# Kernel tuning notes

Measured on AMD Instinct MI355X. Metric: run time of the kernel, lower is better.

Reference implementation:

```python
import jax, jax.numpy as jnp
import numpy as np

B, S, D_MODEL = 1, 1024, 1024
D_CKV, D_CQ = 256, 512
N_HEAD, D_HEAD, D_ROPE = 8, 64, 32


def setup_inputs() -> dict:
    key = jax.random.key(0)
    ks = jax.random.split(key, 12)
    def w(k, shape):
        return jax.random.normal(k, shape, dtype=jnp.float32) * 0.02
    return {
        "x": jax.random.normal(ks[0], (B, S, D_MODEL), dtype=jnp.float32),
        "w_q_idx": w(ks[1], (D_MODEL, N_HEAD * D_HEAD)),
        "w_k_idx": w(ks[2], (D_MODEL, D_HEAD)),
        "w_idx": jnp.ones((N_HEAD,), dtype=jnp.float32),
        "raw_delta": jnp.zeros((D_ROPE // 2,), dtype=jnp.float32),
        "w_dkv": w(ks[3], (D_MODEL, D_CKV)),
        "w_uk": w(ks[4], (D_CKV, N_HEAD * D_HEAD)),
        "w_uv": w(ks[5], (D_CKV, N_HEAD * D_HEAD)),
        "w_dq": w(ks[6], (D_MODEL, D_CQ)),
        "w_uq": w(ks[7], (D_CQ, N_HEAD * D_HEAD)),
        "w_qr": w(ks[8], (D_CQ, N_HEAD * D_ROPE)),
        "w_kr": w(ks[9], (D_MODEL, D_ROPE)),
        "w_out": w(ks[10], (N_HEAD * D_HEAD, D_MODEL)),
        "k_ts": 128,
        "local_window": 64,
    }


def _pope(x, raw_delta, theta):
    # x: (b, L, H, d_rope); positions run along axis 1 (matches torch PoPE)
    delta = -2.0 * jnp.pi * jax.nn.sigmoid(raw_delta)            # (d2,)
    pos = jnp.arange(x.shape[1], dtype=x.dtype)
    ang = pos[None, :, None, None] * theta + delta               # (1, L, 1, d2)
    c, s = jnp.cos(ang), jnp.sin(ang)
    mu1, mu2 = jnp.split(jax.nn.softplus(x), 2, axis=-1)
    return jnp.concatenate((mu1 * c - mu2 * s, mu1 * s + mu2 * c), axis=-1)


def reference(x, w_q_idx, w_k_idx, w_idx, raw_delta, w_dkv, w_uk, w_uv,
              w_dq, w_uq, w_qr, w_kr, w_out, k_ts, local_window):
    b, s, _ = x.shape
    h, dh, dr = N_HEAD, D_HEAD, D_ROPE
    theta = 1.0 / (10000.0 ** (2.0 * jnp.arange(dr // 2, dtype=jnp.float32) / dr))

    # ---- LightningIndexer: per-head relu'd relevance, combined with learned head weights
    qI = (x @ w_q_idx).reshape(b, s, h, dh)
    kI = x @ w_k_idx                                             # (b, s, dh)
    sc = jax.nn.relu(jnp.einsum('bthd,bsd->bths', qI, kI))
    I = jnp.einsum('bths,h->bts', sc, w_idx)

    # ---- TokenSelector: force local window in, mask future out, top-k indices
    qp = jnp.arange(s)[:, None]
    kp = jnp.arange(s)[None, :]
    local = (kp >= qp - local_window + 1) & (kp <= qp)
    causal = kp > qp
    I = jnp.where(local, jnp.inf, I)
    I = jnp.where(causal, -jnp.inf, I)
    k = min(k_ts, s)
    _, idx = jax.lax.top_k(I, k)                                 # (b, s, k) int32

    gather = jax.vmap(lambda t, i: t[i])                         # (s,d),(l,k)->(l,k,d)

    # ---- MLA latent KV, gathered per query
    c_kv = x @ w_dkv                                             # (b, s, d_ckv)
    ckv_sel = gather(c_kv, idx)                                  # (b, s, k, d_ckv)
    key_c = (ckv_sel @ w_uk).reshape(b, s, k, h, dh).transpose(0, 3, 1, 2, 4)
    value = (ckv_sel @ w_uv).reshape(b, s, k, h, dh).transpose(0, 3, 1, 2, 4)

    c_q = x @ w_dq
    query_c = (c_q @ w_uq).reshape(b, s, h, dh).transpose(0, 2, 1, 3)
    query_r = _pope((c_q @ w_qr).reshape(b, s, h, dr), raw_delta, theta).transpose(0, 2, 1, 3)

    # key rope: PoPE applied with positions along the k (selected-token) axis,
    # exactly as the torch code's permute(0,2,1,3) does
    x_sel = gather(x, idx)                                       # (b, s, k, d_model)
    kr = _pope((x_sel @ w_kr).transpose(0, 2, 1, 3), raw_delta, theta).transpose(0, 2, 1, 3)
    key_r = jnp.broadcast_to(kr[:, None], (b, h, s, k, dr))

    query = jnp.concatenate((query_c, query_r), axis=-1)         # (b, h, s, dh+dr)
    keyt = jnp.concatenate((key_c, key_r), axis=-1)              # (b, h, s, k, dh+dr)
    scale = (dh + dr) ** -0.5
    scores = jnp.einsum('bhld,bhlkd->bhlk', query, keyt) * scale
    attn = jax.nn.softmax(scores, axis=-1)
    out = jnp.einsum('bhlk,bhlkd->bhld', attn, value)
    out = out.transpose(0, 2, 1, 3).reshape(b, s, h * dh)
    return out @ w_out
```

## Files before the change

kernel.cpp:

```cpp
#include <hip/hip_runtime.h>
#include <math.h>

#define S_LEN 1024
#define NH 8

typedef __attribute__((ext_vector_type(8))) short bf16x8;
typedef __attribute__((ext_vector_type(4))) float f32x4;

__device__ __forceinline__ float sp_softplus(float x) {
    return fmaxf(x, 0.f) + log1pf(expf(-fabsf(x)));
}

__device__ __forceinline__ unsigned short bfu(float f) {
    unsigned u = __float_as_uint(f);
    unsigned r = (u + 0x7FFFu + ((u >> 16) & 1u)) >> 16;
    return (unsigned short)r;
}

struct FRONT {
    const float *x, *wqidx, *wkidx, *raw_delta, *wuk;
    const float *wdkv, *wdq, *wkr, *wuq, *wqr, *wuv, *wout;
    float *qIP, *kIP, *csc, *css;
    unsigned short *wdkvT, *wdqT, *wkrT, *wuqT, *wqrT, *wuvT, *woutT, *wukb;
};

__global__ __launch_bounds__(256) void front_kernel(FRONT f)
{
    __shared__ float As[2][16][18];
    __shared__ float Bs[2][16][68];
    __shared__ unsigned short tile[64][65];
    int bx = blockIdx.x;
    if (bx < 1152) {
        int gx = bx % 18, gy = bx / 18;
        int half = threadIdx.x >> 7;
        int t = threadIdx.x & 127;
        int u = gx * 2 + half;
        const float* B; float* C;
        int ldb, N, n0, kb;
        if (u < 32) {
            B = f.wqidx; ldb = 512; N = 512;
            C = f.qIP + (long)(u >> 3) * 524288;
            n0 = (u & 7) * 64;
            kb = (u >> 3) * 256;
        } else {
            B = f.wkidx; ldb = 64; N = 64;
            C = f.kIP + (long)(u - 32) * 65536;
            n0 = 0;
            kb = (u - 32) * 256;
        }
        int ke = kb + 256;
        int m0 = gy * 16;
        int ar = t >> 2, ak = t & 3;
        int bk = t >> 3, bn = t & 7;
        int ty = t >> 4, tx = t & 15;

        float4 aN = make_float4(0.f, 0.f, 0.f, 0.f);
        if (t < 64) aN = *(const float4*)(f.x + (long)(m0 + ar) * 1024 + kb + ak * 4);
        float4 b0 = *(const float4*)(B + (long)(kb + bk) * ldb + n0 + bn * 4);
        float4 b1 = *(const float4*)(B + (long)(kb + bk) * ldb + n0 + (bn + 8) * 4);
        float acc[2][4] = {};
        for (int k0 = kb; k0 < ke; k0 += 16) {
            if (t < 64) {
                As[half][ak * 4 + 0][ar] = aN.x;
                As[half][ak * 4 + 1][ar] = aN.y;
                As[half][ak * 4 + 2][ar] = aN.z;
                As[half][ak * 4 + 3][ar] = aN.w;
            }
            *(float4*)&Bs[half][bk][bn * 4] = b0;
            *(float4*)&Bs[half][bk][(bn + 8) * 4] = b1;
            __syncthreads();
            if (k0 + 16 < ke) {
                if (t < 64) aN = *(const float4*)(f.x + (long)(m0 + ar) * 1024 + (k0 + 16) + ak * 4);
                b0 = *(const float4*)(B + (long)(k0 + 16 + bk) * ldb + n0 + bn * 4);
                b1 = *(const float4*)(B + (long)(k0 + 16 + bk) * ldb + n0 + (bn + 8) * 4);
            }
            #pragma unroll
            for (int kk = 0; kk < 16; ++kk) {
                float2 a = *(float2*)&As[half][kk][ty * 2];
                float4 b = *(float4*)&Bs[half][kk][tx * 4];
                acc[0][0] += a.x * b.x; acc[0][1] += a.x * b.y;
                acc[0][2] += a.x * b.z; acc[0][3] += a.x * b.w;
                acc[1][0] += a.y * b.x; acc[1][1] += a.y * b.y;
                acc[1][2] += a.y * b.z; acc[1][3] += a.y * b.w;
            }
            __syncthreads();
        }
        #pragma unroll
        for (int i = 0; i < 2; ++i) {
            float4 v = make_float4(acc[i][0], acc[i][1], acc[i][2], acc[i][3]);
            *(float4*)(C + (long)(m0 + ty * 2 + i) * N + n0 + tx * 4) = v;
        }
    } else if (bx < 1616) {
        int b = bx - 1152;
        const float* srcs[7] = {f.wdkv, f.wdq, f.wkr, f.wuq, f.wqr, f.wuv, f.wout};
        unsigned short* dsts[7] = {f.wdkvT, f.wdqT, f.wkrT, f.wuqT, f.wqrT, f.wuvT, f.woutT};
        const int Ns[7]   = {256, 512, 32, 512, 256, 512, 1024};
        const int Klds[7] = {1024, 1024, 1024, 512, 512, 256, 512};
        const int Ntl[7]  = {4, 8, 1, 8, 4, 8, 16};
        const int bst[8]  = {0, 64, 192, 208, 272, 304, 336, 464};
        int e = 0;
        #pragma unroll
        for (int i = 1; i < 7; ++i) if (b >= bst[i]) e = i;
        int lb = b - bst[e];
        int nt = lb % Ntl[e], kt = lb / Ntl[e];
        const float* src = srcs[e];
        unsigned short* dst = dsts[e];
        int N = Ns[e], Kld = Klds[e];
        int k0 = kt * 64, n0 = nt * 64;
        int t = threadIdx.x;
        int c = t & 63, r4 = t >> 6;
        #pragma unroll
        for (int it = 0; it < 16; ++it) {
            int r = it * 4 + r4;
            float v = (n0 + c < N) ? src[(long)(k0 + r) * N + n0 + c] : 0.f;
            tile[r][c] = bfu(v);
        }
        __syncthreads();
        int wq = t & 7;
        #pragma unroll
        for (int itw = 0; itw < 2; ++itw) {
            int wr = itw * 32 + (t >> 3);
            if (n0 + wr < N) {
                unsigned short v[8];
                #pragma unroll
                for (int j = 0; j < 8; ++j) v[j] = tile[wq * 8 + j][wr];
                *(uint4*)(dst + (long)(n0 + wr) * Kld + k0 + wq * 8) = *(uint4*)v;
            }
        }
    } else if (bx < 1624) {
        int idx = (bx - 1616) * 256 + threadIdx.x;
        int j = idx >> 4, i = idx & 15;
        float rd = f.raw_delta[i];
        float delta = -6.283185307179586f * (1.f / (1.f + expf(-rd)));
        float th = exp2f(-(float)i * 0.83048202372184f);
        float ang = (float)j * th + delta;
        float sv, cv;
        sincosf(ang, &sv, &cv);
        f.csc[idx] = cv;
        f.css[idx] = sv;
    } else {
        int idx = (bx - 1624) * 256 + threadIdx.x;
        f.wukb[idx] = bfu(f.wuk[idx]);
    }
}

struct MFG {
    const float* A[10]; const unsigned short* B[10]; float* C[10];
    int lda[10], ldb[10], ldc[10], K[10], N[10], obf[10];
    int tstart[11]; int ne;
};

__global__ __launch_bounds__(256) void mgemm(MFG mg)
{
    int bx = blockIdx.x, e = 0;
    #pragma unroll
    for (int i = 1; i < 10; ++i) if (i < mg.ne && bx >= mg.tstart[i]) e = i;
    const float* A = mg.A[e];
    const unsigned short* B = mg.B[e];
    float* C = mg.C[e];
    int lda = mg.lda[e], ldb = mg.ldb[e], ldc = mg.ldc[e];
    int K = mg.K[e], N = mg.N[e];
    int m0 = blockIdx.y * 64, n0 = (bx - mg.tstart[e]) * 64;

    __shared__ unsigned short As[64][40];
    __shared__ unsigned short Bs[64][40];
    int t = threadIdx.x;
    int srow = t >> 2, skq = t & 3;
    int wid = t >> 6, l = t & 63;
    int wm = (wid >> 1) * 32, wn = (wid & 1) * 32;
    int fr = l & 15, fk = (l >> 4) * 8;
    bool bok = (n0 + srow) < N;

    f32x4 acc00 = {0.f, 0.f, 0.f, 0.f};
    f32x4 acc01 = {0.f, 0.f, 0.f, 0.f};
    f32x4 acc10 = {0.f, 0.f, 0.f, 0.f};
    f32x4 acc11 = {0.f, 0.f, 0.f, 0.f};

    for (int k0 = 0; k0 < K; k0 += 32) {
        {
            const float* ap = A + (long)(m0 + srow) * lda + k0 + skq * 8;
            float4 v0 = *(const float4*)ap;
            float4 v1 = *(const float4*)(ap + 4);
            unsigned short* d = &As[srow][skq * 8];
            d[0] = bfu(v0.x); d[1] = bfu(v0.y); d[2] = bfu(v0.z); d[3] = bfu(v0.w);
            d[4] = bfu(v1.x); d[5] = bfu(v1.y); d[6] = bfu(v1.z); d[7] = bfu(v1.w);
        }
        {
            uint4 bv = make_uint4(0u, 0u, 0u, 0u);
            if (bok) bv = *(const uint4*)(B + (long)(n0 + srow) * ldb + k0 + skq * 8);
            *(uint4*)&Bs[srow][skq * 8] = bv;
        }
        __syncthreads();
        bf16x8 a0 = *(bf16x8*)&As[wm + fr][fk];
        bf16x8 a1 = *(bf16x8*)&As[wm + 16 + fr][fk];
        bf16x8 b0 = *(bf16x8*)&Bs[wn + fr][fk];
        bf16x8 b1 = *(bf16x8*)&Bs[wn + 16 + fr][fk];
        acc00 = __builtin_amdgcn_mfma_f32_16x16x32_bf16(a0, b0, acc00, 0, 0, 0);
        acc01 = __builtin_amdgcn_mfma_f32_16x16x32_bf16(a0, b1, acc01, 0, 0, 0);
        acc10 = __builtin_amdgcn_mfma_f32_16x16x32_bf16(a1, b0, acc10, 0, 0, 0);
        acc11 = __builtin_amdgcn_mfma_f32_16x16x32_bf16(a1, b1, acc11, 0, 0, 0);
        __syncthreads();
    }
    int crow = (l >> 4) * 4;
    int col0 = n0 + wn + fr, col1 = n0 + wn + 16 + fr;
    if (mg.obf[e]) {
        unsigned short* Cu = (unsigned short*)C;
        if (col0 < N) {
            #pragma unroll
            for (int r = 0; r < 4; ++r) {
                Cu[(long)(m0 + wm + crow + r) * ldc + col0]      = bfu(acc00[r]);
                Cu[(long)(m0 + wm + 16 + crow + r) * ldc + col0] = bfu(acc10[r]);
            }
        }
        if (col1 < N) {
            #pragma unroll
            for (int r = 0; r < 4; ++r) {
                Cu[(long)(m0 + wm + crow + r) * ldc + col1]      = bfu(acc01[r]);
                Cu[(long)(m0 + wm + 16 + crow + r) * ldc + col1] = bfu(acc11[r]);
            }
        }
    } else {
        if (col0 < N) {
            #pragma unroll
            for (int r = 0; r < 4; ++r) {
                C[(long)(m0 + wm + crow + r) * ldc + col0]      = acc00[r];
                C[(long)(m0 + wm + 16 + crow + r) * ldc + col0] = acc10[r];
            }
        }
        if (col1 < N) {
            #pragma unroll
            for (int r = 0; r < 4; ++r) {
                C[(long)(m0 + wm + crow + r) * ldc + col1]      = acc01[r];
                C[(long)(m0 + wm + 16 + crow + r) * ldc + col1] = acc11[r];
            }
        }
    }
}

struct MIDARG {
    const float *qIP, *kIP, *w_idx; float* I;
    const float* qc; const unsigned short* wukb; float* qabs;
    const float *qrp, *raw_delta; float* qrr;
    const float* xkr; float* mu;
};

__global__ __launch_bounds__(256) void mid_kernel(MIDARG g)
{
    __shared__ __align__(16) char smem[26112];
    int b = blockIdx.x;
    int t = threadIdx.x;
    if (b < 512) {
        int sb = b % 16, tb = b / 16;
        if (sb * 64 > tb * 32 + 31) return;
        int t0 = tb * 32, s0 = sb * 64;
        float (*ksT)[68] = (float(*)[68])smem;
        float (*qs)[68]  = (float(*)[68])(smem + 17408);
        {
            int r = t & 63, q = t >> 6;
            #pragma unroll
            for (int u = 0; u < 4; ++u) {
                int c4 = q * 4 + u;
                long off = (long)(s0 + r) * 64 + c4 * 4;
                float4 v = *(const float4*)(g.kIP + off);
                #pragma unroll
                for (int s = 1; s < 4; ++s) {
                    float4 v2 = *(const float4*)(g.kIP + (long)s * 65536 + off);
                    v.x += v2.x; v.y += v2.y; v.z += v2.z; v.w += v2.w;
                }
                ksT[c4 * 4 + 0][r] = v.x;
                ksT[c4 * 4 + 1][r] = v.y;
                ksT[c4 * 4 + 2][r] = v.z;
                ksT[c4 * 4 + 3][r] = v.w;
            }
        }
        int ty = t >> 4, tx = t & 15;
        float accI[2][4] = {};
        for (int h = 0; h < 8; ++h) {
            __syncthreads();
            {
                int r = t >> 3, q = t & 7;
                long base = (long)(t0 + r) * 512 + h * 64;
                #pragma unroll
                for (int half = 0; half < 2; ++half) {
                    long off = base + (q + half * 8) * 4;
                    float4 a = *(const float4*)(g.qIP + off);
                    #pragma unroll
                    for (int s = 1; s < 4; ++s) {
                        float4 a1 = *(const float4*)(g.qIP + (long)s * 524288 + off);
                        a.x += a1.x; a.y += a1.y; a.z += a1.z; a.w += a1.w;
                    }
                    *(float4*)&qs[r][(q + half * 8) * 4] = a;
                }
            }
            __syncthreads();
            float acc[2][4] = {};
            #pragma unroll
            for (int dc = 0; dc < 4; ++dc) {
                float a0[16], a1[16];
                #pragma unroll
                for (int u = 0; u < 4; ++u) {
                    float4 v0 = *(float4*)&qs[ty * 2][dc * 16 + u * 4];
                    float4 v1 = *(float4*)&qs[ty * 2 + 1][dc * 16 + u * 4];
                    a0[u * 4 + 0] = v0.x; a0[u * 4 + 1] = v0.y; a0[u * 4 + 2] = v0.z; a0[u * 4 + 3] = v0.w;
                    a1[u * 4 + 0] = v1.x; a1[u * 4 + 1] = v1.y; a1[u * 4 + 2] = v1.z; a1[u * 4 + 3] = v1.w;
                }
                #pragma unroll
                for (int kk = 0; kk < 16; ++kk) {
                    int d = dc * 16 + kk;
                    float4 bb = *(float4*)&ksT[d][tx * 4];
                    acc[0][0] += a0[kk] * bb.x; acc[0][1] += a0[kk] * bb.y;
                    acc[0][2] += a0[kk] * bb.z; acc[0][3] += a0[kk] * bb.w;
                    acc[1][0] += a1[kk] * bb.x; acc[1][1] += a1[kk] * bb.y;
                    acc[1][2] += a1[kk] * bb.z; acc[1][3] += a1[kk] * bb.w;
                }
            }
            float wh = g.w_idx[h];
            #pragma unroll
            for (int i = 0; i < 2; ++i)
                #pragma unroll
                for (int j = 0; j < 4; ++j)
                    accI[i][j] += wh * fmaxf(acc[i][j], 0.f);
        }
        #pragma unroll
        for (int i = 0; i < 2; ++i) {
            float4 v = make_float4(accI[i][0], accI[i][1], accI[i][2], accI[i][3]);
            *(float4*)&g.I[(long)(t0 + ty * 2 + i) * 1024 + s0 + tx * 4] = v;
        }
    } else if (b < 1024) {
        int lb = b - 512;
        int h = lb >> 6, rem = lb & 63;
        int n0 = (rem >> 4) * 64, m0 = (rem & 15) * 64;
        const float* A = g.qc + h * 64;
        const unsigned short* B = g.wukb + h * 64;
        float* C = g.qabs + h * 256;
        unsigned short (*As)[40] = (unsigned short(*)[40])smem;
        unsigned short (*Bs)[40] = (unsigned short(*)[40])(smem + 5120);
        int srow = t >> 2, skq = t & 3;
        int wid = t >> 6, l = t & 63;
        int wm = (wid >> 1) * 32, wn = (wid & 1) * 32;
        int fr = l & 15, fk = (l >> 4) * 8;
        f32x4 acc00 = {0.f, 0.f, 0.f, 0.f};
        f32x4 acc01 = {0.f, 0.f, 0.f, 0.f};
        f32x4 acc10 = {0.f, 0.f, 0.f, 0.f};
        f32x4 acc11 = {0.f, 0.f, 0.f, 0.f};
        for (int k0 = 0; k0 < 64; k0 += 32) {
            {
                const float* ap = A + (long)(m0 + srow) * 512 + k0 + skq * 8;
                float4 v0 = *(const float4*)ap;
                float4 v1 = *(const float4*)(ap + 4);
                unsigned short* d = &As[srow][skq * 8];
                d[0] = bfu(v0.x); d[1] = bfu(v0.y); d[2] = bfu(v0.z); d[3] = bfu(v0.w);
                d[4] = bfu(v1.x); d[5] = bfu(v1.y); d[6] = bfu(v1.z); d[7] = bfu(v1.w);
            }
            {
                uint4 bv = *(const uint4*)(B + (long)(n0 + srow) * 512 + k0 + skq * 8);
                *(uint4*)&Bs[srow][skq * 8] = bv;
            }
            __syncthreads();
            bf16x8 a0 = *(bf16x8*)&As[wm + fr][fk];
            bf16x8 a1 = *(bf16x8*)&As[wm + 16 + fr][fk];
            bf16x8 b0 = *(bf16x8*)&Bs[wn + fr][fk];
            bf16x8 b1 = *(bf16x8*)&Bs[wn + 16 + fr][fk];
            acc00 = __builtin_amdgcn_mfma_f32_16x16x32_bf16(a0, b0, acc00, 0, 0, 0);
            acc01 = __builtin_amdgcn_mfma_f32_16x16x32_bf16(a0, b1, acc01, 0, 0, 0);
            acc10 = __builtin_amdgcn_mfma_f32_16x16x32_bf16(a1, b0, acc10, 0, 0, 0);
            acc11 = __builtin_amdgcn_mfma_f32_16x16x32_bf16(a1, b1, acc11, 0, 0, 0);
            __syncthreads();
        }
        int crow = (l >> 4) * 4;
        int col0 = n0 + wn + fr, col1 = n0 + wn + 16 + fr;
        #pragma unroll
        for (int r = 0; r < 4; ++r) {
            C[(long)(m0 + wm + crow + r) * 2048 + col0]      = acc00[r];
            C[(long)(m0 + wm + 16 + crow + r) * 2048 + col0] = acc10[r];
            C[(long)(m0 + wm + crow + r) * 2048 + col1]      = acc01[r];
            C[(long)(m0 + wm + 16 + crow + r) * 2048 + col1] = acc11[r];
        }
    } else if (b < 1536) {
        int tq = (b - 1024) * 2 + (t >> 7);
        int tt = t & 127;
        int h = tt >> 4, i = tt & 15;
        float rd = g.raw_delta[i];
        float delta = -6.283185307179586f * (1.f / (1.f + expf(-rd)));
        float th = exp2f(-(float)i * 0.83048202372184f);
        float ang = (float)tq * th + delta;
        float sv, cv;
        sincosf(ang, &sv, &cv);
        float m1 = sp_softplus(g.qrp[tq * 256 + h * 32 + i]);
        float m2 = sp_softplus(g.qrp[tq * 256 + h * 32 + 16 + i]);
        g.qrr[tq * 256 + h * 32 + i]      = m1 * cv - m2 * sv;
        g.qrr[tq * 256 + h * 32 + 16 + i] = m1 * sv + m2 * cv;
    } else {
        int i = (b - 1536) * 256 + t;
        g.mu[i] = sp_softplus(g.xkr[i]);
    }
}

__global__ __launch_bounds__(256) void topk_kernel(
    const float* __restrict__ I, int* __restrict__ idxout)
{
    int t = blockIdx.x * 4 + (threadIdx.x >> 6);
    int lane = threadIdx.x & 63;
    int smin = max(0, t - 63);
    int w = min(64, t + 1);
    if (lane < w) idxout[t * 128 + lane] = smin + lane;
    for (int q = t + 1 + lane; q < 128; q += 64)
        idxout[t * 128 + q] = q;
    int f = max(0, t - 63);
    int m = min(f, 64);
    if (m == 0) return;
    const float* row = I + (long)t * 1024;

    unsigned long long key[16];
    #pragma unroll
    for (int g4 = 0; g4 < 4; ++g4) {
        float4 v = *(const float4*)(row + lane * 16 + g4 * 4);
        float vv[4] = {v.x, v.y, v.z, v.w};
        #pragma unroll
        for (int j = 0; j < 4; ++j) {
            int s = lane * 16 + g4 * 4 + j;
            unsigned long long k = 0ull;
            if (s < f) {
                unsigned u = __float_as_uint(vv[j]);
                unsigned ou = (u & 0x80000000u) ? ~u : (u | 0x80000000u);
                k = ((unsigned long long)ou << 32) | (0xFFFFFFFFu - (unsigned)s);
            }
            key[g4 * 4 + j] = k;
        }
    }

    #pragma unroll
    for (int km = 1; km <= 10; ++km) {
        #pragma unroll
        for (int jm = km - 1; jm >= 0; --jm) {
            if (jm >= 4) {
                int lmask = 1 << (jm - 4);
                #pragma unroll
                for (int r = 0; r < 16; ++r) {
                    unsigned long long other = __shfl_xor(key[r], lmask, 64);
                    int i = lane * 16 + r;
                    bool keep_max = (((i & (1 << km)) == 0) == ((i & (1 << jm)) == 0));
                    unsigned long long mx = key[r] > other ? key[r] : other;
                    unsigned long long mn = key[r] > other ? other : key[r];
                    key[r] = keep_max ? mx : mn;
                }
            } else {
                int rmask = 1 << jm;
                #pragma unroll
                for (int r = 0; r < 16; ++r) {
                    if ((r & rmask) == 0) {
                        int r2 = r | rmask;
                        int i = lane * 16 + r;
                        bool keep_max_low = ((i & (1 << km)) == 0);
                        unsigned long long a = key[r], b = key[r2];
                        unsigned long long mx = a > b ? a : b;
                        unsigned long long mn = a > b ? b : a;
                        key[r]  = keep_max_low ? mx : mn;
                        key[r2] = keep_max_low ? mn : mx;
                    }
                }
            }
        }
    }

    if (lane < 4) {
        #pragma unroll
        for (int r = 0; r < 16; ++r) {
            int e = lane * 16 + r;
            if (e < m) {
                int s = (int)(0xFFFFFFFFu - (unsigned)(key[r] & 0xFFFFFFFFull));
                idxout[t * 128 + w + e] = s;
            }
        }
    }
}

__global__ __launch_bounds__(256) void attn_kernel(
    const float* __restrict__ qabs, const float* __restrict__ qrr,
    const unsigned short* __restrict__ ckvb, const float* __restrict__ mu,
    const float* __restrict__ csc, const float* __restrict__ css,
    const int* __restrict__ idxb, float* __restrict__ olat)
{
    __shared__ float sc[8][68];
    __shared__ float hs[16];
    __shared__ int idx_s[128];

    int t = blockIdx.x, tid = threadIdx.x;
    int w = tid >> 6, l = tid & 63;
    const float scale = 0.10206207261596575f;

    if (tid < 128) idx_s[tid] = idxb[t * 128 + tid];

    int hrow = l & 15;
    int kslice = (l >> 4) * 8;
    int hpv = l >> 3;
    int c8 = w * 64 + (l & 7) * 8;

    float mrun0 = -INFINITY, mrun1 = -INFINITY;
    float lrun0 = 0.f, lrun1 = 0.f;
    float acc0 = 0, acc1 = 0, acc2 = 0, acc3 = 0;
    float acc4 = 0, acc5 = 0, acc6 = 0, acc7 = 0;

    __syncthreads();

    #pragma unroll
    for (int chunk = 0; chunk < 2; ++chunk) {
        if (chunk) __syncthreads();

        int r = w * 16 + hrow;
        int src = idx_s[chunk * 64 + r];
        int jglob = chunk * 64 + r;
        f32x4 st = {0.f, 0.f, 0.f, 0.f};
        #pragma unroll
        for (int ks = 0; ks < 8; ++ks) {
            bf16x8 af = *(const bf16x8*)(ckvb + (long)src * 256 + ks * 32 + kslice);
            bf16x8 qf = {0, 0, 0, 0, 0, 0, 0, 0};
            if (hrow < 8) {
                const float* qp = qabs + (long)t * 2048 + hrow * 256 + ks * 32 + kslice;
                float4 a = *(const float4*)qp;
                float4 b = *(const float4*)(qp + 4);
                unsigned short qq[8];
                qq[0] = bfu(a.x * scale); qq[1] = bfu(a.y * scale);
                qq[2] = bfu(a.z * scale); qq[3] = bfu(a.w * scale);
                qq[4] = bfu(b.x * scale); qq[5] = bfu(b.y * scale);
                qq[6] = bfu(b.z * scale); qq[7] = bfu(b.w * scale);
                qf = *(bf16x8*)qq;
            }
            st = __builtin_amdgcn_mfma_f32_16x16x32_bf16(af, qf, st, 0, 0, 0);
        }
        {
            int i15 = kslice & 15;
            bool lo = kslice < 16;
            float4 m1a = *(const float4*)(mu + src * 32 + i15);
            float4 m1b = *(const float4*)(mu + src * 32 + i15 + 4);
            float4 m2a = *(const float4*)(mu + src * 32 + 16 + i15);
            float4 m2b = *(const float4*)(mu + src * 32 + 16 + i15 + 4);
            float4 ca = *(const float4*)(csc + jglob * 16 + i15);
            float4 cb = *(const float4*)(csc + jglob * 16 + i15 + 4);
            float4 sa = *(const float4*)(css + jglob * 16 + i15);
            float4 sb = *(const float4*)(css + jglob * 16 + i15 + 4);
            unsigned short hh[8];
            hh[0] = bfu(lo ? m1a.x * ca.x - m2a.x * sa.x : m1a.x * sa.x + m2a.x * ca.x);
            hh[1] = bfu(lo ? m1a.y * ca.y - m2a.y * sa.y : m1a.y * sa.y + m2a.y * ca.y);
            hh[2] = bfu(lo ? m1a.z * ca.z - m2a.z * sa.z : m1a.z * sa.z + m2a.z * ca.z);
            hh[3] = bfu(lo ? m1a.w * ca.w - m2a.w * sa.w : m1a.w * sa.w + m2a.w * ca.w);
            hh[4] = bfu(lo ? m1b.x * cb.x - m2b.x * sb.x : m1b.x * sb.x + m2b.x * cb.x);
            hh[5] = bfu(lo ? m1b.y * cb.y - m2b.y * sb.y : m1b.y * sb.y + m2b.y * cb.y);
            hh[6] = bfu(lo ? m1b.z * cb.z - m2b.z * sb.z : m1b.z * sb.z + m2b.z * cb.z);
            hh[7] = bfu(lo ? m1b.w * cb.w - m2b.w * sb.w : m1b.w * sb.w + m2b.w * cb.w);
            bf16x8 af = *(bf16x8*)hh;
            bf16x8 qf = {0, 0, 0, 0, 0, 0, 0, 0};
            if (hrow < 8) {
                const float* qp = qrr + (long)t * 256 + hrow * 32 + kslice;
                float4 a = *(const float4*)qp;
                float4 b = *(const float4*)(qp + 4);
                unsigned short qq[8];
                qq[0] = bfu(a.x * scale); qq[1] = bfu(a.y * scale);
                qq[2] = bfu(a.z * scale); qq[3] = bfu(a.w * scale);
                qq[4] = bfu(b.x * scale); qq[5] = bfu(b.y * scale);
                qq[6] = bfu(b.z * scale); qq[7] = bfu(b.w * scale);
                qf = *(bf16x8*)qq;
            }
            st = __builtin_amdgcn_mfma_f32_16x16x32_bf16(af, qf, st, 0, 0, 0);
        }
        {
            int srow2 = w * 16 + (l >> 4) * 4;
            if (hrow < 8) {
                #pragma unroll
                for (int rr = 0; rr < 4; ++rr) sc[hrow][srow2 + rr] = st[rr];
            }
        }
        __syncthreads();

        float rh0, rh1;
        {
            int h = 2 * w;
            float v = sc[h][l];
            float mx = v;
            #pragma unroll
            for (int off = 32; off > 0; off >>= 1) mx = fmaxf(mx, __shfl_xor(mx, off));
            float mnew = fmaxf(mrun0, mx);
            float p = expf(v - mnew);
            float ps = p;
            #pragma unroll
            for (int off = 32; off > 0; off >>= 1) ps += __shfl_xor(ps, off);
            rh0 = expf(mrun0 - mnew);
            lrun0 = lrun0 * rh0 + ps;
            mrun0 = mnew;
            sc[h][l] = p;
        }
        {
            int h = 2 * w + 1;
            float v = sc[h][l];
            float mx = v;
            #pragma unroll
            for (int off = 32; off > 0; off >>= 1) mx = fmaxf(mx, __shfl_xor(mx, off));
            float mnew = fmaxf(mrun1, mx);
            float p = expf(v - mnew);
            float ps = p;
            #pragma unroll
            for (int off = 32; off > 0; off >>= 1) ps += __shfl_xor(ps, off);
            rh1 = expf(mrun1 - mnew);
            lrun1 = lrun1 * rh1 + ps;
            mrun1 = mnew;
            sc[h][l] = p;
        }
        if (l == 0) {
            hs[2 * w] = rh0;
            hs[2 * w + 1] = rh1;
            if (chunk == 1) {
                hs[8 + 2 * w] = lrun0;
                hs[8 + 2 * w + 1] = lrun1;
            }
        }
        __syncthreads();

        float rsel = hs[hpv];
        acc0 *= rsel; acc1 *= rsel; acc2 *= rsel; acc3 *= rsel;
        acc4 *= rsel; acc5 *= rsel; acc6 *= rsel; acc7 *= rsel;
        #pragma unroll 8
        for (int j = 0; j < 64; ++j) {
            float p = sc[hpv][j];
            int srcj = idx_s[chunk * 64 + j];
            uint4 vv = *(const uint4*)(ckvb + (long)srcj * 256 + c8);
            acc0 += p * __uint_as_float(vv.x << 16);
            acc1 += p * __uint_as_float(vv.x & 0xffff0000u);
            acc2 += p * __uint_as_float(vv.y << 16);
            acc3 += p * __uint_as_float(vv.y & 0xffff0000u);
            acc4 += p * __uint_as_float(vv.z << 16);
            acc5 += p * __uint_as_float(vv.z & 0xffff0000u);
            acc6 += p * __uint_as_float(vv.w << 16);
            acc7 += p * __uint_as_float(vv.w & 0xffff0000u);
        }
    }

    float inv = 1.f / hs[8 + hpv];
    float* op = olat + (long)t * 2048 + hpv * 256 + c8;
    *(float4*)op       = make_float4(acc0 * inv, acc1 * inv, acc2 * inv, acc3 * inv);
    *(float4*)(op + 4) = make_float4(acc4 * inv, acc5 * inv, acc6 * inv, acc7 * inv);
}

extern "C" void kernel_launch(void* const* d_in, const int* in_sizes, int n_in,
                              void* d_out, int out_size, void* d_ws, size_t ws_size,
                              hipStream_t stream)
{
    const float* x         = (const float*)d_in[0];
    const float* w_q_idx   = (const float*)d_in[1];
    const float* w_k_idx   = (const float*)d_in[2];
    const float* w_idx     = (const float*)d_in[3];
    const float* raw_delta = (const float*)d_in[4];
    const float* w_dkv     = (const float*)d_in[5];
    const float* w_uk      = (const float*)d_in[6];
    const float* w_uv      = (const float*)d_in[7];
    const float* w_dq      = (const float*)d_in[8];
    const float* w_uq      = (const float*)d_in[9];
    const float* w_qr      = (const float*)d_in[10];
    const float* w_kr      = (const float*)d_in[11];
    const float* w_out     = (const float*)d_in[12];
    (void)in_sizes; (void)n_in; (void)out_size; (void)ws_size;
    float* out = (float*)d_out;

    float* ws = (float*)d_ws;
    unsigned short* ckvb = (unsigned short*)ws;   ws += 131072;
    float* cq    = ws;        ws += 1024 * 512;
    float* xkr   = ws;        ws += 1024 * 32;
    float* qrp   = ws;        ws += 1024 * 256;
    float* qrr   = ws;        ws += 1024 * 256;
    float* qc    = ws;        ws += 1024 * 512;
    float* qabs  = ws;        ws += 1024 * 2048;
    float* Ibuf  = ws;        ws += 1024 * 1024;
    int*   idxb  = (int*)ws;  ws += 1024 * 128;
    float* olat  = ws;        ws += 1024 * 2048;
    float* outh  = ws;        ws += 1024 * 512;
    float* mu    = ws;        ws += 1024 * 32;
    float* cscb  = ws;        ws += 128 * 16;
    float* cssb  = ws;        ws += 128 * 16;
    unsigned short* wdkvT = (unsigned short*)ws;  ws += 131072;
    unsigned short* wdqT  = (unsigned short*)ws;  ws += 262144;
    unsigned short* wkrT  = (unsigned short*)ws;  ws += 16384;
    unsigned short* wuqT  = (unsigned short*)ws;  ws += 131072;
    unsigned short* wqrT  = (unsigned short*)ws;  ws += 65536;
    unsigned short* wuvT  = (unsigned short*)ws;  ws += 65536;
    unsigned short* woutT = (unsigned short*)ws;  ws += 262144;
    unsigned short* wukb  = (unsigned short*)ws;  ws += 65536;
    float* part  = ws;        ws += 2359296;
    float* qIP = part;
    float* kIP = part + 2097152;

    {
        FRONT f{};
        f.x = x; f.wqidx = w_q_idx; f.wkidx = w_k_idx; f.raw_delta = raw_delta; f.wuk = w_uk;
        f.wdkv = w_dkv; f.wdq = w_dq; f.wkr = w_kr; f.wuq = w_uq; f.wqr = w_qr;
        f.wuv = w_uv; f.wout = w_out;
        f.qIP = qIP; f.kIP = kIP; f.csc = cscb; f.css = cssb;
        f.wdkvT = wdkvT; f.wdqT = wdqT; f.wkrT = wkrT; f.wuqT = wuqT;
        f.wqrT = wqrT; f.wuvT = wuvT; f.woutT = woutT; f.wukb = wukb;
        front_kernel<<<dim3(2136), dim3(256), 0, stream>>>(f);
    }

    {
        MFG m{};
        for (int i = 0; i < 3; ++i) { m.A[i]=x; m.lda[i]=1024; m.K[i]=1024; }
        m.B[0]=wdkvT; m.C[0]=(float*)ckvb; m.ldb[0]=1024; m.ldc[0]=256; m.N[0]=256; m.obf[0]=1;
        m.B[1]=wdqT;  m.C[1]=cq;           m.ldb[1]=1024; m.ldc[1]=512; m.N[1]=512;
        m.B[2]=wkrT;  m.C[2]=xkr;          m.ldb[2]=1024; m.ldc[2]=32;  m.N[2]=32;
        m.tstart[0]=0; m.tstart[1]=4; m.tstart[2]=12; m.tstart[3]=13;
        m.ne = 3;
        mgemm<<<dim3(13, 16), dim3(256), 0, stream>>>(m);
    }

    {
        MFG m{};
        for (int i = 0; i < 2; ++i) { m.A[i]=cq; m.lda[i]=512; m.K[i]=512; }
        m.B[0]=wuqT; m.C[0]=qc;  m.ldb[0]=512; m.ldc[0]=512; m.N[0]=512;
        m.B[1]=wqrT; m.C[1]=qrp; m.ldb[1]=512; m.ldc[1]=256; m.N[1]=256;
        m.tstart[0]=0; m.tstart[1]=8; m.tstart[2]=12;
        m.ne = 2;
        mgemm<<<dim3(12, 16), dim3(256), 0, stream>>>(m);
    }

    {
        MIDARG g{};
        g.qIP = qIP; g.kIP = kIP; g.w_idx = w_idx; g.I = Ibuf;
        g.qc = qc; g.wukb = wukb; g.qabs = qabs;
        g.qrp = qrp; g.raw_delta = raw_delta; g.qrr = qrr;
        g.xkr = xkr; g.mu = mu;
        mid_kernel<<<dim3(1664), dim3(256), 0, stream>>>(g);
    }

    topk_kernel<<<dim3(256), dim3(256), 0, stream>>>(Ibuf, idxb);

    attn_kernel<<<dim3(1024), dim3(256), 0, stream>>>(qabs, qrr, ckvb, mu, cscb, cssb, idxb, olat);

    {
        MFG m{};
        for (int h = 0; h < 8; ++h) {
            m.A[h] = olat + h * 256;      m.lda[h] = 2048; m.K[h] = 256;
            m.B[h] = wuvT + h * 64 * 256; m.ldb[h] = 256;
            m.C[h] = outh + h * 64;       m.ldc[h] = 512;  m.N[h] = 64;
            m.tstart[h] = h;
        }
        m.tstart[8] = 8;
        m.ne = 8;
        mgemm<<<dim3(8, 16), dim3(256), 0, stream>>>(m);
    }

    {
        MFG m{};
        m.A[0] = outh;  m.lda[0] = 512; m.K[0] = 512;
        m.B[0] = woutT; m.ldb[0] = 512;
        m.C[0] = out;   m.ldc[0] = 1024; m.N[0] = 1024;
        m.tstart[0] = 0; m.tstart[1] = 16;
        m.ne = 1;
        mgemm<<<dim3(16, 16), dim3(256), 0, stream>>>(m);
    }
}
```

Measured before the change: 195.9 us.

## Split attention over two key chunks per token with separate combine kernel

The attention kernel now launches one block per (token, 64-key chunk) rather than looping over both chunks in a single block. Each block writes an unnormalized partial accumulator plus its max and sum, and a new combine kernel merges the two partials flash-decoding style. This doubles the number of blocks to expose more parallelism and removes the serial dependency between chunks. In exchange it adds an extra launch and a round trip of partial results through global memory, and the workspace is reorganized so the partial buffers alias dead intermediate buffers.

```diff
diff --git a/kernel.cpp b/kernel.cpp
--- a/kernel.cpp
+++ b/kernel.cpp
@@ -479,165 +479,173 @@
     const float* __restrict__ qabs, const float* __restrict__ qrr,
     const unsigned short* __restrict__ ckvb, const float* __restrict__ mu,
     const float* __restrict__ csc, const float* __restrict__ css,
-    const int* __restrict__ idxb, float* __restrict__ olat)
+    const int* __restrict__ idxb, float* __restrict__ pacc,
+    float* __restrict__ pml)
 {
     __shared__ float sc[8][68];
-    __shared__ float hs[16];
-    __shared__ int idx_s[128];
-
-    int t = blockIdx.x, tid = threadIdx.x;
+    __shared__ float hl[16];
+    __shared__ int idx_s[64];
+
+    int bx = blockIdx.x, tid = threadIdx.x;
+    int t = bx >> 1, chunk = bx & 1;
     int w = tid >> 6, l = tid & 63;
     const float scale = 0.10206207261596575f;
 
-    if (tid < 128) idx_s[tid] = idxb[t * 128 + tid];
+    if (tid < 64) idx_s[tid] = idxb[t * 128 + chunk * 64 + tid];
 
     int hrow = l & 15;
     int kslice = (l >> 4) * 8;
     int hpv = l >> 3;
     int c8 = w * 64 + (l & 7) * 8;
 
-    float mrun0 = -INFINITY, mrun1 = -INFINITY;
-    float lrun0 = 0.f, lrun1 = 0.f;
+    __syncthreads();
+
+    int r = w * 16 + hrow;
+    int src = idx_s[r];
+    int jglob = chunk * 64 + r;
+    f32x4 st = {0.f, 0.f, 0.f, 0.f};
+    #pragma unroll
+    for (int ks = 0; ks < 8; ++ks) {
+        bf16x8 af = *(const bf16x8*)(ckvb + (long)src * 256 + ks * 32 + kslice);
+        bf16x8 qf = {0, 0, 0, 0, 0, 0, 0, 0};
+        if (hrow < 8) {
+            const float* qp = qabs + (long)t * 2048 + hrow * 256 + ks * 32 + kslice;
+            float4 a = *(const float4*)qp;
+            float4 b = *(const float4*)(qp + 4);
+            unsigned short qq[8];
+            qq[0] = bfu(a.x * scale); qq[1] = bfu(a.y * scale);
+            qq[2] = bfu(a.z * scale); qq[3] = bfu(a.w * scale);
+            qq[4] = bfu(b.x * scale); qq[5] = bfu(b.y * scale);
+            qq[6] = bfu(b.z * scale); qq[7] = bfu(b.w * scale);
+            qf = *(bf16x8*)qq;
+        }
+        st = __builtin_amdgcn_mfma_f32_16x16x32_bf16(af, qf, st, 0, 0, 0);
+    }
+    {
+        int i15 = kslice & 15;
+        bool lo = kslice < 16;
+        float4 m1a = *(const float4*)(mu + src * 32 + i15);
+        float4 m1b = *(const float4*)(mu + src * 32 + i15 + 4);
+        float4 m2a = *(const float4*)(mu + src * 32 + 16 + i15);
+        float4 m2b = *(const float4*)(mu + src * 32 + 16 + i15 + 4);
+        float4 ca = *(const float4*)(csc + jglob * 16 + i15);
+        float4 cb = *(const float4*)(csc + jglob * 16 + i15 + 4);
+        float4 sa = *(const float4*)(css + jglob * 16 + i15);
+        float4 sb = *(const float4*)(css + jglob * 16 + i15 + 4);
+        unsigned short hh[8];
+        hh[0] = bfu(lo ? m1a.x * ca.x - m2a.x * sa.x : m1a.x * sa.x + m2a.x * ca.x);
+        hh[1] = bfu(lo ? m1a.y * ca.y - m2a.y * sa.y : m1a.y * sa.y + m2a.y * ca.y);
+        hh[2] = bfu(lo ? m1a.z * ca.z - m2a.z * sa.z : m1a.z * sa.z + m2a.z * ca.z);
+        hh[3] = bfu(lo ? m1a.w * ca.w - m2a.w * sa.w : m1a.w * sa.w + m2a.w * ca.w);
+        hh[4] = bfu(lo ? m1b.x * cb.x - m2b.x * sb.x : m1b.x * sb.x + m2b.x * cb.x);
+        hh[5] = bfu(lo ? m1b.y * cb.y - m2b.y * sb.y : m1b.y * sb.y + m2b.y * cb.y);
+        hh[6] = bfu(lo ? m1b.z * cb.z - m2b.z * sb.z : m1b.z * sb.z + m2b.z * cb.z);
+        hh[7] = bfu(lo ? m1b.w * cb.w - m2b.w * sb.w : m1b.w * sb.w + m2b.w * cb.w);
+        bf16x8 af = *(bf16x8*)hh;
+        bf16x8 qf = {0, 0, 0, 0, 0, 0, 0, 0};
+        if (hrow < 8) {
+            const float* qp = qrr + (long)t * 256 + hrow * 32 + kslice;
+            float4 a = *(const float4*)qp;
+            float4 b = *(const float4*)(qp + 4);
+            unsigned short qq[8];
+            qq[0] = bfu(a.x * scale); qq[1] = bfu(a.y * scale);
+            qq[2] = bfu(a.z * scale); qq[3] = bfu(a.w * scale);
+            qq[4] = bfu(b.x * scale); qq[5] = bfu(b.y * scale);
+            qq[6] = bfu(b.z * scale); qq[7] = bfu(b.w * scale);
+            qf = *(bf16x8*)qq;
+        }
+        st = __builtin_amdgcn_mfma_f32_16x16x32_bf16(af, qf, st, 0, 0, 0);
+    }
+    {
+        int srow2 = w * 16 + (l >> 4) * 4;
+        if (hrow < 8) {
+            #pragma unroll
+            for (int rr = 0; rr < 4; ++rr) sc[hrow][srow2 + rr] = st[rr];
+        }
+    }
+    __syncthreads();
+
+    {
+        int h = 2 * w;
+        float v = sc[h][l];
+        float mx = v;
+        #pragma unroll
+        for (int off = 32; off > 0; off >>= 1) mx = fmaxf(mx, __shfl_xor(mx, off));
+        float p = expf(v - mx);
+        float ps = p;
+        #pragma unroll
+        for (int off = 32; off > 0; off >>= 1) ps += __shfl_xor(ps, off);
+        sc[h][l] = p;
+        if (l == 0) { hl[h] = mx; hl[8 + h] = ps; }
+    }
+    {
+        int h = 2 * w + 1;
+        float v = sc[h][l];
+        float mx = v;
+        #pragma unroll
+        for (int off = 32; off > 0; off >>= 1) mx = fmaxf(mx, __shfl_xor(mx, off));
+        float p = expf(v - mx);
+        float ps = p;
+        #pragma unroll
+        for (int off = 32; off > 0; off >>= 1) ps += __shfl_xor(ps, off);
+        sc[h][l] = p;
+        if (l == 0) { hl[h] = mx; hl[8 + h] = ps; }
+    }
+    __syncthreads();
+
     float acc0 = 0, acc1 = 0, acc2 = 0, acc3 = 0;
     float acc4 = 0, acc5 = 0, acc6 = 0, acc7 = 0;
-
-    __syncthreads();
-
-    #pragma unroll
-    for (int chunk = 0; chunk < 2; ++chunk) {
-        if (chunk) __syncthreads();
-
-        int r = w * 16 + hrow;
-        int src = idx_s[chunk * 64 + r];
-        int jglob = chunk * 64 + r;
-        f32x4 st = {0.f, 0.f, 0.f, 0.f};
-        #pragma unroll
-        for (int ks = 0; ks < 8; ++ks) {
-            bf16x8 af = *(const bf16x8*)(ckvb + (long)src * 256 + ks * 32 + kslice);
-            bf16x8 qf = {0, 0, 0, 0, 0, 0, 0, 0};
-            if (hrow < 8) {
-                const float* qp = qabs + (long)t * 2048 + hrow * 256 + ks * 32 + kslice;
-                float4 a = *(const float4*)qp;
-                float4 b = *(const float4*)(qp + 4);
-                unsigned short qq[8];
-                qq[0] = bfu(a.x * scale); qq[1] = bfu(a.y * scale);
-                qq[2] = bfu(a.z * scale); qq[3] = bfu(a.w * scale);
-                qq[4] = bfu(b.x * scale); qq[5] = bfu(b.y * scale);
-                qq[6] = bfu(b.z * scale); qq[7] = bfu(b.w * scale);
-                qf = *(bf16x8*)qq;
-            }
-            st = __builtin_amdgcn_mfma_f32_16x16x32_bf16(af, qf, st, 0, 0, 0);
-        }
-        {
-            int i15 = kslice & 15;
-            bool lo = kslice < 16;
-            float4 m1a = *(const float4*)(mu + src * 32 + i15);
-            float4 m1b = *(const float4*)(mu + src * 32 + i15 + 4);
-            float4 m2a = *(const float4*)(mu + src * 32 + 16 + i15);
-            float4 m2b = *(const float4*)(mu + src * 32 + 16 + i15 + 4);
-            float4 ca = *(const float4*)(csc + jglob * 16 + i15);
-            float4 cb = *(const float4*)(csc + jglob * 16 + i15 + 4);
-            float4 sa = *(const float4*)(css + jglob * 16 + i15);
-            float4 sb = *(const float4*)(css + jglob * 16 + i15 + 4);
-            unsigned short hh[8];
-            hh[0] = bfu(lo ? m1a.x * ca.x - m2a.x * sa.x : m1a.x * sa.x + m2a.x * ca.x);
-            hh[1] = bfu(lo ? m1a.y * ca.y - m2a.y * sa.y : m1a.y * sa.y + m2a.y * ca.y);
-            hh[2] = bfu(lo ? m1a.z * ca.z - m2a.z * sa.z : m1a.z * sa.z + m2a.z * ca.z);
-            hh[3] = bfu(lo ? m1a.w * ca.w - m2a.w * sa.w : m1a.w * sa.w + m2a.w * ca.w);
-            hh[4] = bfu(lo ? m1b.x * cb.x - m2b.x * sb.x : m1b.x * sb.x + m2b.x * cb.x);
-            hh[5] = bfu(lo ? m1b.y * cb.y - m2b.y * sb.y : m1b.y * sb.y + m2b.y * cb.y);
-            hh[6] = bfu(lo ? m1b.z * cb.z - m2b.z * sb.z : m1b.z * sb.z + m2b.z * cb.z);
-            hh[7] = bfu(lo ? m1b.w * cb.w - m2b.w * sb.w : m1b.w * sb.w + m2b.w * cb.w);
-            bf16x8 af = *(bf16x8*)hh;
-            bf16x8 qf = {0, 0, 0, 0, 0, 0, 0, 0};
-            if (hrow < 8) {
-                const float* qp = qrr + (long)t * 256 + hrow * 32 + kslice;
-                float4 a = *(const float4*)qp;
-                float4 b = *(const float4*)(qp + 4);
-                unsigned short qq[8];
-                qq[0] = bfu(a.x * scale); qq[1] = bfu(a.y * scale);
-                qq[2] = bfu(a.z * scale); qq[3] = bfu(a.w * scale);
-                qq[4] = bfu(b.x * scale); qq[5] = bfu(b.y * scale);
-                qq[6] = bfu(b.z * scale); qq[7] = bfu(b.w * scale);
-                qf = *(bf16x8*)qq;
-            }
-            st = __builtin_amdgcn_mfma_f32_16x16x32_bf16(af, qf, st, 0, 0, 0);
-        }
-        {
-            int srow2 = w * 16 + (l >> 4) * 4;
-            if (hrow < 8) {
-                #pragma unroll
-                for (int rr = 0; rr < 4; ++rr) sc[hrow][srow2 + rr] = st[rr];
-            }
-        }
-        __syncthreads();
-
-        float rh0, rh1;
-        {
-            int h = 2 * w;
-            float v = sc[h][l];
-            float mx = v;
-            #pragma unroll
-            for (int off = 32; off > 0; off >>= 1) mx = fmaxf(mx, __shfl_xor(mx, off));
-            float mnew = fmaxf(mrun0, mx);
-            float p = expf(v - mnew);
-            float ps = p;
-            #pragma unroll
-            for (int off = 32; off > 0; off >>= 1) ps += __shfl_xor(ps, off);
-            rh0 = expf(mrun0 - mnew);
-            lrun0 = lrun0 * rh0 + ps;
-            mrun0 = mnew;
-            sc[h][l] = p;
-        }
-        {
-            int h = 2 * w + 1;
-            float v = sc[h][l];
-            float mx = v;
-            #pragma unroll
-            for (int off = 32; off > 0; off >>= 1) mx = fmaxf(mx, __shfl_xor(mx, off));
-            float mnew = fmaxf(mrun1, mx);
-            float p = expf(v - mnew);
-            float ps = p;
-            #pragma unroll
-            for (int off = 32; off > 0; off >>= 1) ps += __shfl_xor(ps, off);
-            rh1 = expf(mrun1 - mnew);
-            lrun1 = lrun1 * rh1 + ps;
-            mrun1 = mnew;
-            sc[h][l] = p;
-        }
-        if (l == 0) {
-            hs[2 * w] = rh0;
-            hs[2 * w + 1] = rh1;
-            if (chunk == 1) {
-                hs[8 + 2 * w] = lrun0;
-                hs[8 + 2 * w + 1] = lrun1;
-            }
-        }
-        __syncthreads();
-
-        float rsel = hs[hpv];
-        acc0 *= rsel; acc1 *= rsel; acc2 *= rsel; acc3 *= rsel;
-        acc4 *= rsel; acc5 *= rsel; acc6 *= rsel; acc7 *= rsel;
-        #pragma unroll 8
-        for (int j = 0; j < 64; ++j) {
-            float p = sc[hpv][j];
-            int srcj = idx_s[chunk * 64 + j];
-            uint4 vv = *(const uint4*)(ckvb + (long)srcj * 256 + c8);
-            acc0 += p * __uint_as_float(vv.x << 16);
-            acc1 += p * __uint_as_float(vv.x & 0xffff0000u);
-            acc2 += p * __uint_as_float(vv.y << 16);
-            acc3 += p * __uint_as_float(vv.y & 0xffff0000u);
-            acc4 += p * __uint_as_float(vv.z << 16);
-            acc5 += p * __uint_as_float(vv.z & 0xffff0000u);
-            acc6 += p * __uint_as_float(vv.w << 16);
-            acc7 += p * __uint_as_float(vv.w & 0xffff0000u);
-        }
-    }
-
-    float inv = 1.f / hs[8 + hpv];
-    float* op = olat + (long)t * 2048 + hpv * 256 + c8;
-    *(float4*)op       = make_float4(acc0 * inv, acc1 * inv, acc2 * inv, acc3 * inv);
-    *(float4*)(op + 4) = make_float4(acc4 * inv, acc5 * inv, acc6 * inv, acc7 * inv);
+    #pragma unroll 8
+    for (int j = 0; j < 64; ++j) {
+        float p = sc[hpv][j];
+        int srcj = idx_s[j];
+        uint4 vv = *(const uint4*)(ckvb + (long)srcj * 256 + c8);
+        acc0 += p * __uint_as_float(vv.x << 16);
+        acc1 += p * __uint_as_float(vv.x & 0xffff0000u);
+        acc2 += p * __uint_as_float(vv.y << 16);
+        acc3 += p * __uint_as_float(vv.y & 0xffff0000u);
+        acc4 += p * __uint_as_float(vv.z << 16);
+        acc5 += p * __uint_as_float(vv.z & 0xffff0000u);
+        acc6 += p * __uint_as_float(vv.w << 16);
+        acc7 += p * __uint_as_float(vv.w & 0xffff0000u);
+    }
+
+    float* op = pacc + (long)bx * 2048 + hpv * 256 + c8;
+    *(float4*)op       = make_float4(acc0, acc1, acc2, acc3);
+    *(float4*)(op + 4) = make_float4(acc4, acc5, acc6, acc7);
+    if (tid < 16) pml[bx * 16 + tid] = hl[tid];
+}
+
+__global__ __launch_bounds__(256) void attn_combine(
+    const float* __restrict__ pacc, const float* __restrict__ pml,
+    float* __restrict__ olat)
+{
+    int t = blockIdx.x, tid = threadIdx.x;
+    int idx = tid * 8;
+    int h = idx >> 8;
+    float m0 = pml[(2 * t) * 16 + h];
+    float m1 = pml[(2 * t + 1) * 16 + h];
+    float l0 = pml[(2 * t) * 16 + 8 + h];
+    float l1 = pml[(2 * t + 1) * 16 + 8 + h];
+    float m = fmaxf(m0, m1);
+    float r0 = expf(m0 - m), r1 = expf(m1 - m);
+    float inv = 1.f / (l0 * r0 + l1 * r1);
+    const float4* a0 = (const float4*)(pacc + (long)(2 * t) * 2048 + idx);
+    const float4* a1 = (const float4*)(pacc + (long)(2 * t + 1) * 2048 + idx);
+    float4 v0 = a0[0], u0 = a0[1];
+    float4 v1 = a1[0], u1 = a1[1];
+    float4 o0, o1;
+    o0.x = (v0.x * r0 + v1.x * r1) * inv;
+    o0.y = (v0.y * r0 + v1.y * r1) * inv;
+    o0.z = (v0.z * r0 + v1.z * r1) * inv;
+    o0.w = (v0.w * r0 + v1.w * r1) * inv;
+    o1.x = (u0.x * r0 + u1.x * r1) * inv;
+    o1.y = (u0.y * r0 + u1.y * r1) * inv;
+    o1.z = (u0.z * r0 + u1.z * r1) * inv;
+    o1.w = (u0.w * r0 + u1.w * r1) * inv;
+    float4* op = (float4*)(olat + (long)t * 2048 + idx);
+    op[0] = o0;
+    op[1] = o1;
 }
 
 extern "C" void kernel_launch(void* const* d_in, const int* in_sizes, int n_in,
@@ -662,30 +670,32 @@
 
     float* ws = (float*)d_ws;
     unsigned short* ckvb = (unsigned short*)ws;   ws += 131072;
-    float* cq    = ws;        ws += 1024 * 512;
-    float* xkr   = ws;        ws += 1024 * 32;
-    float* qrp   = ws;        ws += 1024 * 256;
-    float* qrr   = ws;        ws += 1024 * 256;
-    float* qc    = ws;        ws += 1024 * 512;
-    float* qabs  = ws;        ws += 1024 * 2048;
-    float* Ibuf  = ws;        ws += 1024 * 1024;
-    int*   idxb  = (int*)ws;  ws += 1024 * 128;
-    float* olat  = ws;        ws += 1024 * 2048;
-    float* outh  = ws;        ws += 1024 * 512;
-    float* mu    = ws;        ws += 1024 * 32;
-    float* cscb  = ws;        ws += 128 * 16;
-    float* cssb  = ws;        ws += 128 * 16;
-    unsigned short* wdkvT = (unsigned short*)ws;  ws += 131072;
-    unsigned short* wdqT  = (unsigned short*)ws;  ws += 262144;
-    unsigned short* wkrT  = (unsigned short*)ws;  ws += 16384;
-    unsigned short* wuqT  = (unsigned short*)ws;  ws += 131072;
-    unsigned short* wqrT  = (unsigned short*)ws;  ws += 65536;
+    float* qabs  = ws;        ws += 2097152;
+    float* qrr   = ws;        ws += 262144;
+    float* mu    = ws;        ws += 32768;
+    float* cscb  = ws;        ws += 2048;
+    float* cssb  = ws;        ws += 2048;
+    int*   idxb  = (int*)ws;  ws += 131072;
+    float* olat  = ws;        ws += 2097152;
+    float* outh  = ws;        ws += 524288;
     unsigned short* wuvT  = (unsigned short*)ws;  ws += 65536;
     unsigned short* woutT = (unsigned short*)ws;  ws += 262144;
-    unsigned short* wukb  = (unsigned short*)ws;  ws += 65536;
-    float* part  = ws;        ws += 2359296;
-    float* qIP = part;
-    float* kIP = part + 2097152;
+    float* uni = ws;
+    float* cq    = uni;
+    float* xkr   = uni + 524288;
+    float* qrp   = uni + 557056;
+    float* qc    = uni + 819200;
+    float* Ibuf  = uni + 1343488;
+    unsigned short* wdkvT = (unsigned short*)(uni + 2392064);
+    unsigned short* wdqT  = (unsigned short*)(uni + 2523136);
+    unsigned short* wkrT  = (unsigned short*)(uni + 2785280);
+    unsigned short* wuqT  = (unsigned short*)(uni + 2801664);
+    unsigned short* wqrT  = (unsigned short*)(uni + 2932736);
+    unsigned short* wukb  = (unsigned short*)(uni + 2998272);
+    float* qIP = uni + 3063808;
+    float* kIP = uni + 5160960;
+    float* pacc = uni;
+    float* pml  = uni + 4194304;
 
     {
         FRONT f{};
@@ -730,7 +740,9 @@
 
     topk_kernel<<<dim3(256), dim3(256), 0, stream>>>(Ibuf, idxb);
 
-    attn_kernel<<<dim3(1024), dim3(256), 0, stream>>>(qabs, qrr, ckvb, mu, cscb, cssb, idxb, olat);
+    attn_kernel<<<dim3(2048), dim3(256), 0, stream>>>(qabs, qrr, ckvb, mu, cscb, cssb, idxb, pacc, pml);
+
+    attn_combine<<<dim3(1024), dim3(256), 0, stream>>>(pacc, pml, olat);
 
     {
         MFG m{};
```

New measurement: 202.1 us. +3.2%, slower.
